# Kernel optimization log

Hardware: AMD Instinct MI355X
Metric: run time of the kernel (lower is better)

## Reference

```python
import jax, jax.numpy as jnp
import numpy as np

N_NODES = 50000
N_EDGES = 600000
IN_DIM = 128
OUT_DIM = 128
LN_EPS = 1e-5


def setup_inputs() -> dict:
    key = jax.random.key(0)
    ks = jax.random.split(key, 8)
    feat = jax.random.normal(ks[0], (N_NODES, IN_DIM), dtype=jnp.float32)
    src = jax.random.randint(ks[1], (N_EDGES,), 0, N_NODES, dtype=jnp.int32)
    dst = jax.random.randint(ks[2], (N_EDGES,), 0, N_NODES, dtype=jnp.int32)
    s = 1.0 / np.sqrt(IN_DIM)
    fc_w = jax.random.uniform(ks[3], (IN_DIM, OUT_DIM), jnp.float32, -s, s)
    fc_b = jax.random.uniform(ks[4], (OUT_DIM,), jnp.float32, -s, s)
    res_w = jax.random.uniform(ks[5], (IN_DIM, OUT_DIM), jnp.float32, -s, s)
    ln_g = jnp.ones((OUT_DIM,), jnp.float32)
    ln_b = jnp.zeros((OUT_DIM,), jnp.float32)
    return {"feat": feat, "src": src, "dst": dst, "fc_w": fc_w,
            "fc_b": fc_b, "res_w": res_w, "ln_g": ln_g, "ln_b": ln_b}


def _deg_norm(idx, n, dtype):
    # degree per node computed from edge endpoint list, clamp(min=1)^-0.5
    deg = jax.ops.segment_sum(jnp.ones(idx.shape, dtype), idx, num_segments=n)
    return jax.lax.rsqrt(jnp.maximum(deg, 1.0))


def _layernorm(x, g, b):
    mu = jnp.mean(x, axis=-1, keepdims=True)
    var = jnp.mean(jnp.square(x - mu), axis=-1, keepdims=True)
    return (x - mu) * jax.lax.rsqrt(var + LN_EPS) * g + b


def reference(feat, src, dst, fc_w, fc_b, res_w, ln_g, ln_b):
    n = feat.shape[0]
    out_norm = _deg_norm(src, n, feat.dtype)  # out-degrees (source norm)
    in_norm = _deg_norm(dst, n, feat.dtype)   # in-degrees (dest norm)
    h = feat * out_norm[:, None]
    # copy_src + sum: gather source features along edges, scatter-add to dst
    agg = jax.ops.segment_sum(h[src], dst, num_segments=n)  # [N, in_dim]
    rst = agg @ fc_w + fc_b
    rst = rst * in_norm[:, None]
    rst = rst + feat @ res_w
    return jax.nn.relu(_layernorm(rst, ln_g, ln_b))
```

## Files before the change

### kernel.cpp

```cpp
#include <hip/hip_runtime.h>

#define N_NODES 50000
#define N_EDGES 600000
#define DIM 128
#define LN_EPS 1e-5f
#define ELL_CAP 64

#define OFF_AGGBF    0
#define OFF_FEATBF   3200000
#define OFF_DEGOUT   6400000
#define OFF_DEGIN    6450000
#define OFF_WTFC     6500000
#define OFF_WTRES    6508192

typedef __attribute__((ext_vector_type(8))) short bf16x8;
typedef __attribute__((ext_vector_type(4))) float f32x4;

__device__ __forceinline__ unsigned int f2bf(float f) {
    unsigned int u = __float_as_uint(f);
    return (u + 0x7FFFu + ((u >> 16) & 1u)) >> 16;
}
__device__ __forceinline__ float bf_lo(unsigned int u) { return __uint_as_float(u << 16); }
__device__ __forceinline__ float bf_hi(unsigned int u) { return __uint_as_float(u & 0xFFFF0000u); }

__global__ void k_prep(const float4* __restrict__ feat, uint2* __restrict__ featbf,
                       unsigned int* __restrict__ degs,
                       const float* __restrict__ fc_w, const float* __restrict__ res_w,
                       unsigned int* __restrict__ wt_fc, unsigned int* __restrict__ wt_res) {
    int gid = blockIdx.x * blockDim.x + threadIdx.x;
    if (gid < N_NODES * DIM / 4) {
        float4 v = feat[gid];
        uint2 o;
        o.x = f2bf(v.x) | (f2bf(v.y) << 16);
        o.y = f2bf(v.z) | (f2bf(v.w) << 16);
        featbf[gid] = o;
    }
    if (gid < 2 * N_NODES) {
        degs[gid] = 0u;
    } else if (gid < 2 * N_NODES + 2 * DIM * (DIM / 2)) {
        int i = gid - 2 * N_NODES;
        int m = i >> 13;
        int r = i & 8191;
        int c = r >> 6;
        int kw = r & 63;
        const float* W = m ? res_w : fc_w;
        unsigned int* O = m ? wt_res : wt_fc;
        float a = W[(size_t)(2 * kw) * DIM + c];
        float b = W[(size_t)(2 * kw + 1) * DIM + c];
        O[c * (DIM / 2) + kw] = f2bf(a) | (f2bf(b) << 16);
    }
}

__global__ void k_count_scatter(const int* __restrict__ src, const int* __restrict__ dst,
                                unsigned int* deg_out, unsigned int* deg_in,
                                unsigned short* __restrict__ ell) {
    int e = blockIdx.x * blockDim.x + threadIdx.x;
    if (e < N_EDGES) {
        int s = src[e], d = dst[e];
        atomicAdd(&deg_out[s], 1u);
        unsigned int ofs = atomicAdd(&deg_in[d], 1u);
        if (ofs < ELL_CAP)
            ell[(size_t)d * ELL_CAP + ofs] = (unsigned short)s;
    }
}

__global__ void k_agg(const unsigned int* __restrict__ featbf,
                      const unsigned int* __restrict__ deg_in,
                      const unsigned int* __restrict__ deg_out,
                      const unsigned short* __restrict__ ell,
                      unsigned int* __restrict__ aggbf) {
    int wid  = (blockIdx.x * blockDim.x + threadIdx.x) >> 6;
    int lane = threadIdx.x & 63;
    if (wid >= N_NODES) return;
    int deg = (int)deg_in[wid];
    if (deg > ELL_CAP) deg = ELL_CAP;
    int   myid = 0;
    float myw  = 0.f;
    if (lane < deg) {
        myid = (int)ell[(size_t)wid * ELL_CAP + lane];
        myw  = rsqrtf(fmaxf((float)deg_out[myid], 1.0f));
    }
    float a0 = 0.f, a1 = 0.f, b0 = 0.f, b1 = 0.f;
    int j = 0;
    for (; j + 3 < deg; j += 4) {
        int   s0 = __shfl(myid, j, 64),     s1 = __shfl(myid, j + 1, 64);
        int   s2 = __shfl(myid, j + 2, 64), s3 = __shfl(myid, j + 3, 64);
        float w0 = __shfl(myw, j, 64),      w1 = __shfl(myw, j + 1, 64);
        float w2 = __shfl(myw, j + 2, 64),  w3 = __shfl(myw, j + 3, 64);
        unsigned int u0 = featbf[(size_t)s0 * 64 + lane];
        unsigned int u1 = featbf[(size_t)s1 * 64 + lane];
        unsigned int u2 = featbf[(size_t)s2 * 64 + lane];
        unsigned int u3 = featbf[(size_t)s3 * 64 + lane];
        a0 = fmaf(w0, bf_lo(u0), a0);  a1 = fmaf(w0, bf_hi(u0), a1);
        b0 = fmaf(w1, bf_lo(u1), b0);  b1 = fmaf(w1, bf_hi(u1), b1);
        a0 = fmaf(w2, bf_lo(u2), a0);  a1 = fmaf(w2, bf_hi(u2), a1);
        b0 = fmaf(w3, bf_lo(u3), b0);  b1 = fmaf(w3, bf_hi(u3), b1);
    }
    for (; j < deg; ++j) {
        int   sa = __shfl(myid, j, 64);
        float wa = __shfl(myw, j, 64);
        unsigned int ua = featbf[(size_t)sa * 64 + lane];
        a0 = fmaf(wa, bf_lo(ua), a0);
        a1 = fmaf(wa, bf_hi(ua), a1);
    }
    float inn = rsqrtf(fmaxf((float)deg, 1.0f));
    a0 = (a0 + b0) * inn;
    a1 = (a1 + b1) * inn;
    aggbf[(size_t)wid * 64 + lane] = f2bf(a0) | (f2bf(a1) << 16);
}

__launch_bounds__(256)
__global__ void k_gemm(const unsigned short* __restrict__ aggbf,
                       const unsigned short* __restrict__ featbf,
                       const unsigned short* __restrict__ wt_fc,
                       const unsigned short* __restrict__ wt_res,
                       const float* __restrict__ fc_b,
                       const unsigned int* __restrict__ deg_in,
                       const float* __restrict__ ln_g, const float* __restrict__ ln_b,
                       float* __restrict__ out) {
    int tid  = threadIdx.x;
    int wave = tid >> 6;
    int lane = tid & 63;
    int fr   = lane & 15;
    int kg   = lane >> 4;
    int row0 = blockIdx.x * 64 + wave * 16;

    f32x4 acc[8];
#pragma unroll
    for (int n = 0; n < 8; n++) acc[n] = (f32x4)0.f;

    int arow = row0 + fr;
#pragma unroll
    for (int pass = 0; pass < 2; ++pass) {
        const unsigned short* X  = pass ? featbf : aggbf;
        const unsigned short* WT = pass ? wt_res : wt_fc;
#pragma unroll
        for (int ks = 0; ks < 4; ++ks) {
            bf16x8 a = *(const bf16x8*)&X[(size_t)arow * DIM + ks * 32 + kg * 8];
#pragma unroll
            for (int n = 0; n < 8; n++) {
                bf16x8 b = *(const bf16x8*)&WT[(size_t)(n * 16 + fr) * DIM + ks * 32 + kg * 8];
                acc[n] = __builtin_amdgcn_mfma_f32_16x16x32_bf16(a, b, acc[n], 0, 0, 0);
            }
        }
    }

    float bia[8], g[8], bb[8];
#pragma unroll
    for (int n = 0; n < 8; n++) {
        int col = n * 16 + fr;
        bia[n] = fc_b[col]; g[n] = ln_g[col]; bb[n] = ln_b[col];
    }
#pragma unroll
    for (int j = 0; j < 4; j++) {
        int row = row0 + kg * 4 + j;
        bool ok = row < N_NODES;
        float inn = ok ? rsqrtf(fmaxf((float)deg_in[row], 1.0f)) : 0.f;
        float x[8], s = 0.f, ss = 0.f;
#pragma unroll
        for (int n = 0; n < 8; n++) {
            x[n] = acc[n][j] + inn * bia[n];
            s += x[n];
            ss = fmaf(x[n], x[n], ss);
        }
#pragma unroll
        for (int m = 1; m < 16; m <<= 1) {
            s  += __shfl_xor(s, m, 64);
            ss += __shfl_xor(ss, m, 64);
        }
        float mu   = s * (1.f / 128.f);
        float var  = ss * (1.f / 128.f) - mu * mu;
        float rstd = rsqrtf(var + LN_EPS);
        if (ok) {
#pragma unroll
            for (int n = 0; n < 8; n++) {
                float o = fmaxf((x[n] - mu) * rstd * g[n] + bb[n], 0.f);
                out[(size_t)row * DIM + n * 16 + fr] = o;
            }
        }
    }
}

extern "C" void kernel_launch(void* const* d_in, const int* in_sizes, int n_in,
                              void* d_out, int out_size, void* d_ws, size_t ws_size,
                              hipStream_t stream) {
    const float* feat  = (const float*)d_in[0];
    const int*   src   = (const int*)d_in[1];
    const int*   dst   = (const int*)d_in[2];
    const float* fc_w  = (const float*)d_in[3];
    const float* fc_b  = (const float*)d_in[4];
    const float* res_w = (const float*)d_in[5];
    const float* ln_g  = (const float*)d_in[6];
    const float* ln_b  = (const float*)d_in[7];
    float* out = (float*)d_out;

    unsigned int* ws_u = (unsigned int*)d_ws;

    unsigned int*   aggbf    = ws_u + OFF_AGGBF;
    unsigned int*   featbf   = ws_u + OFF_FEATBF;
    unsigned int*   deg_out  = ws_u + OFF_DEGOUT;
    unsigned int*   deg_in   = ws_u + OFF_DEGIN;
    unsigned int*   wt_fc    = ws_u + OFF_WTFC;
    unsigned int*   wt_res   = ws_u + OFF_WTRES;
    unsigned short* ell      = (unsigned short*)d_out;

    k_prep<<<(N_NODES * DIM / 4 + 255) / 256, 256, 0, stream>>>(
        (const float4*)feat, (uint2*)featbf, deg_out, fc_w, res_w, wt_fc, wt_res);
    k_count_scatter<<<(N_EDGES + 255) / 256, 256, 0, stream>>>(src, dst, deg_out,
                                                               deg_in, ell);
    {
        long long tot_threads = (long long)N_NODES * 64;
        int blocks = (int)((tot_threads + 255) / 256);
        k_agg<<<blocks, 256, 0, stream>>>(featbf, deg_in, deg_out, ell, aggbf);
    }
    k_gemm<<<(N_NODES + 63) / 64, 256, 0, stream>>>(
        (const unsigned short*)aggbf, (const unsigned short*)featbf,
        (const unsigned short*)wt_fc, (const unsigned short*)wt_res,
        fc_b, deg_in, ln_g, ln_b, out);
}
```

Measured before the change: 213.9 us.

## Fuse aggregation into GEMM via LDS and merge edge scatter with feature conversion

The per-node gather-aggregation now runs inside the GEMM kernel: each wave aggregates its 16 rows into a swizzled LDS tile, which then feeds the fc MFMA directly. This removes the aggbf round trip through global memory and one kernel launch. The bf16 feature conversion is moved into the edge-counting kernel as separate blocks, and each edge thread now handles two edges. The cost is fewer waves doing aggregation (16 rows per wave, done serially), which can reduce the memory-level parallelism available to hide gather latency.

New measurement: 228.5 us. +6.8%, slower.

```diff
diff --git a/kernel.cpp b/kernel.cpp
--- a/kernel.cpp
+++ b/kernel.cpp
@@ -2,16 +2,20 @@
 
 #define N_NODES 50000
 #define N_EDGES 600000
+#define HALF_E  300000
 #define DIM 128
 #define LN_EPS 1e-5f
 #define ELL_CAP 64
 
-#define OFF_AGGBF    0
-#define OFF_FEATBF   3200000
-#define OFF_DEGOUT   6400000
-#define OFF_DEGIN    6450000
-#define OFF_WTFC     6500000
-#define OFF_WTRES    6508192
+#define OFF_FEATBF   0
+#define OFF_DEGOUT   3200000
+#define OFF_DEGIN    3250000
+#define OFF_WTFC     3300000
+#define OFF_WTRES    3308192
+
+#define EDGE_BLOCKS  ((HALF_E + 255) / 256)
+#define CONV_TASKS   (N_NODES * DIM / 4)
+#define CONV_BLOCKS  ((CONV_TASKS + 255) / 256)
 
 typedef __attribute__((ext_vector_type(8))) short bf16x8;
 typedef __attribute__((ext_vector_type(4))) float f32x4;
@@ -23,18 +27,10 @@
 __device__ __forceinline__ float bf_lo(unsigned int u) { return __uint_as_float(u << 16); }
 __device__ __forceinline__ float bf_hi(unsigned int u) { return __uint_as_float(u & 0xFFFF0000u); }
 
-__global__ void k_prep(const float4* __restrict__ feat, uint2* __restrict__ featbf,
-                       unsigned int* __restrict__ degs,
-                       const float* __restrict__ fc_w, const float* __restrict__ res_w,
-                       unsigned int* __restrict__ wt_fc, unsigned int* __restrict__ wt_res) {
+__global__ void k_pre(unsigned int* __restrict__ degs,
+                      const float* __restrict__ fc_w, const float* __restrict__ res_w,
+                      unsigned int* __restrict__ wt_fc, unsigned int* __restrict__ wt_res) {
     int gid = blockIdx.x * blockDim.x + threadIdx.x;
-    if (gid < N_NODES * DIM / 4) {
-        float4 v = feat[gid];
-        uint2 o;
-        o.x = f2bf(v.x) | (f2bf(v.y) << 16);
-        o.y = f2bf(v.z) | (f2bf(v.w) << 16);
-        featbf[gid] = o;
-    }
     if (gid < 2 * N_NODES) {
         degs[gid] = 0u;
     } else if (gid < 2 * N_NODES + 2 * DIM * (DIM / 2)) {
@@ -51,97 +47,118 @@
     }
 }
 
-__global__ void k_count_scatter(const int* __restrict__ src, const int* __restrict__ dst,
-                                unsigned int* deg_out, unsigned int* deg_in,
-                                unsigned short* __restrict__ ell) {
-    int e = blockIdx.x * blockDim.x + threadIdx.x;
-    if (e < N_EDGES) {
-        int s = src[e], d = dst[e];
-        atomicAdd(&deg_out[s], 1u);
-        unsigned int ofs = atomicAdd(&deg_in[d], 1u);
-        if (ofs < ELL_CAP)
-            ell[(size_t)d * ELL_CAP + ofs] = (unsigned short)s;
-    }
-}
-
-__global__ void k_agg(const unsigned int* __restrict__ featbf,
-                      const unsigned int* __restrict__ deg_in,
-                      const unsigned int* __restrict__ deg_out,
-                      const unsigned short* __restrict__ ell,
-                      unsigned int* __restrict__ aggbf) {
-    int wid  = (blockIdx.x * blockDim.x + threadIdx.x) >> 6;
-    int lane = threadIdx.x & 63;
-    if (wid >= N_NODES) return;
-    int deg = (int)deg_in[wid];
-    if (deg > ELL_CAP) deg = ELL_CAP;
-    int   myid = 0;
-    float myw  = 0.f;
-    if (lane < deg) {
-        myid = (int)ell[(size_t)wid * ELL_CAP + lane];
-        myw  = rsqrtf(fmaxf((float)deg_out[myid], 1.0f));
-    }
-    float a0 = 0.f, a1 = 0.f, b0 = 0.f, b1 = 0.f;
-    int j = 0;
-    for (; j + 3 < deg; j += 4) {
-        int   s0 = __shfl(myid, j, 64),     s1 = __shfl(myid, j + 1, 64);
-        int   s2 = __shfl(myid, j + 2, 64), s3 = __shfl(myid, j + 3, 64);
-        float w0 = __shfl(myw, j, 64),      w1 = __shfl(myw, j + 1, 64);
-        float w2 = __shfl(myw, j + 2, 64),  w3 = __shfl(myw, j + 3, 64);
-        unsigned int u0 = featbf[(size_t)s0 * 64 + lane];
-        unsigned int u1 = featbf[(size_t)s1 * 64 + lane];
-        unsigned int u2 = featbf[(size_t)s2 * 64 + lane];
-        unsigned int u3 = featbf[(size_t)s3 * 64 + lane];
-        a0 = fmaf(w0, bf_lo(u0), a0);  a1 = fmaf(w0, bf_hi(u0), a1);
-        b0 = fmaf(w1, bf_lo(u1), b0);  b1 = fmaf(w1, bf_hi(u1), b1);
-        a0 = fmaf(w2, bf_lo(u2), a0);  a1 = fmaf(w2, bf_hi(u2), a1);
-        b0 = fmaf(w3, bf_lo(u3), b0);  b1 = fmaf(w3, bf_hi(u3), b1);
-    }
-    for (; j < deg; ++j) {
-        int   sa = __shfl(myid, j, 64);
-        float wa = __shfl(myw, j, 64);
-        unsigned int ua = featbf[(size_t)sa * 64 + lane];
-        a0 = fmaf(wa, bf_lo(ua), a0);
-        a1 = fmaf(wa, bf_hi(ua), a1);
-    }
-    float inn = rsqrtf(fmaxf((float)deg, 1.0f));
-    a0 = (a0 + b0) * inn;
-    a1 = (a1 + b1) * inn;
-    aggbf[(size_t)wid * 64 + lane] = f2bf(a0) | (f2bf(a1) << 16);
+__global__ void k_main(const int* __restrict__ src, const int* __restrict__ dst,
+                       unsigned int* deg_out, unsigned int* deg_in,
+                       unsigned short* __restrict__ ell,
+                       const float4* __restrict__ feat, uint2* __restrict__ featbf) {
+    int b = blockIdx.x;
+    if (b < EDGE_BLOCKS) {
+        int g = b * 256 + threadIdx.x;
+        if (g < HALF_E) {
+            int s0 = src[g],          d0 = dst[g];
+            int s1 = src[g + HALF_E], d1 = dst[g + HALF_E];
+            atomicAdd(&deg_out[s0], 1u);
+            atomicAdd(&deg_out[s1], 1u);
+            unsigned int o0 = atomicAdd(&deg_in[d0], 1u);
+            unsigned int o1 = atomicAdd(&deg_in[d1], 1u);
+            if (o0 < ELL_CAP) ell[(size_t)d0 * ELL_CAP + o0] = (unsigned short)s0;
+            if (o1 < ELL_CAP) ell[(size_t)d1 * ELL_CAP + o1] = (unsigned short)s1;
+        }
+    } else {
+        int g = (b - EDGE_BLOCKS) * 256 + threadIdx.x;
+        if (g < CONV_TASKS) {
+            float4 v = feat[g];
+            uint2 o;
+            o.x = f2bf(v.x) | (f2bf(v.y) << 16);
+            o.y = f2bf(v.z) | (f2bf(v.w) << 16);
+            featbf[g] = o;
+        }
+    }
 }
 
 __launch_bounds__(256)
-__global__ void k_gemm(const unsigned short* __restrict__ aggbf,
-                       const unsigned short* __restrict__ featbf,
-                       const unsigned short* __restrict__ wt_fc,
-                       const unsigned short* __restrict__ wt_res,
-                       const float* __restrict__ fc_b,
-                       const unsigned int* __restrict__ deg_in,
-                       const float* __restrict__ ln_g, const float* __restrict__ ln_b,
-                       float* __restrict__ out) {
+__global__ void k_agg_gemm(const unsigned int* __restrict__ featbf,
+                           const unsigned int* __restrict__ deg_in,
+                           const unsigned int* __restrict__ deg_out,
+                           const unsigned short* __restrict__ ell,
+                           const unsigned short* __restrict__ wt_fc,
+                           const unsigned short* __restrict__ wt_res,
+                           const float* __restrict__ fc_b,
+                           const float* __restrict__ ln_g, const float* __restrict__ ln_b,
+                           float* __restrict__ out) {
+    __shared__ unsigned int lds[4 * 16 * 64];
     int tid  = threadIdx.x;
     int wave = tid >> 6;
     int lane = tid & 63;
     int fr   = lane & 15;
     int kg   = lane >> 4;
     int row0 = blockIdx.x * 64 + wave * 16;
+    unsigned int* wlds = &lds[wave * 1024];
+
+    for (int n = 0; n < 16; ++n) {
+        int row = row0 + n;
+        int tdeg = 0;
+        if (row < N_NODES) tdeg = (int)deg_in[row];
+        int deg = tdeg > ELL_CAP ? ELL_CAP : tdeg;
+        int   myid = 0;
+        float myw  = 0.f;
+        if (lane < deg) {
+            myid = (int)ell[(size_t)row * ELL_CAP + lane];
+            myw  = rsqrtf(fmaxf((float)deg_out[myid], 1.0f));
+        }
+        float a0 = 0.f, a1 = 0.f, c0 = 0.f, c1 = 0.f;
+        int j = 0;
+        for (; j + 3 < deg; j += 4) {
+            int   s0 = __shfl(myid, j, 64),     s1 = __shfl(myid, j + 1, 64);
+            int   s2 = __shfl(myid, j + 2, 64), s3 = __shfl(myid, j + 3, 64);
+            float w0 = __shfl(myw, j, 64),      w1 = __shfl(myw, j + 1, 64);
+            float w2 = __shfl(myw, j + 2, 64),  w3 = __shfl(myw, j + 3, 64);
+            unsigned int u0 = featbf[(size_t)s0 * 64 + lane];
+            unsigned int u1 = featbf[(size_t)s1 * 64 + lane];
+            unsigned int u2 = featbf[(size_t)s2 * 64 + lane];
+            unsigned int u3 = featbf[(size_t)s3 * 64 + lane];
+            a0 = fmaf(w0, bf_lo(u0), a0);  a1 = fmaf(w0, bf_hi(u0), a1);
+            c0 = fmaf(w1, bf_lo(u1), c0);  c1 = fmaf(w1, bf_hi(u1), c1);
+            a0 = fmaf(w2, bf_lo(u2), a0);  a1 = fmaf(w2, bf_hi(u2), a1);
+            c0 = fmaf(w3, bf_lo(u3), c0);  c1 = fmaf(w3, bf_hi(u3), c1);
+        }
+        for (; j < deg; ++j) {
+            int   sa = __shfl(myid, j, 64);
+            float wa = __shfl(myw, j, 64);
+            unsigned int ua = featbf[(size_t)sa * 64 + lane];
+            a0 = fmaf(wa, bf_lo(ua), a0);
+            a1 = fmaf(wa, bf_hi(ua), a1);
+        }
+        float inn = rsqrtf(fmaxf((float)tdeg, 1.0f));
+        a0 = (a0 + c0) * inn;
+        a1 = (a1 + c1) * inn;
+        wlds[n * 64 + ((((lane >> 2) + n) & 15) << 2) + (lane & 3)] =
+            f2bf(a0) | (f2bf(a1) << 16);
+    }
+    __syncthreads();
 
     f32x4 acc[8];
 #pragma unroll
     for (int n = 0; n < 8; n++) acc[n] = (f32x4)0.f;
 
+#pragma unroll
+    for (int ks = 0; ks < 4; ++ks) {
+        bf16x8 a = *(const bf16x8*)&wlds[fr * 64 + (((ks * 4 + kg + fr) & 15) << 2)];
+#pragma unroll
+        for (int n = 0; n < 8; n++) {
+            bf16x8 bfr = *(const bf16x8*)&wt_fc[(size_t)(n * 16 + fr) * DIM + ks * 32 + kg * 8];
+            acc[n] = __builtin_amdgcn_mfma_f32_16x16x32_bf16(a, bfr, acc[n], 0, 0, 0);
+        }
+    }
     int arow = row0 + fr;
-#pragma unroll
-    for (int pass = 0; pass < 2; ++pass) {
-        const unsigned short* X  = pass ? featbf : aggbf;
-        const unsigned short* WT = pass ? wt_res : wt_fc;
-#pragma unroll
-        for (int ks = 0; ks < 4; ++ks) {
-            bf16x8 a = *(const bf16x8*)&X[(size_t)arow * DIM + ks * 32 + kg * 8];
-#pragma unroll
-            for (int n = 0; n < 8; n++) {
-                bf16x8 b = *(const bf16x8*)&WT[(size_t)(n * 16 + fr) * DIM + ks * 32 + kg * 8];
-                acc[n] = __builtin_amdgcn_mfma_f32_16x16x32_bf16(a, b, acc[n], 0, 0, 0);
-            }
+    if (arow >= N_NODES) arow = N_NODES - 1;
+#pragma unroll
+    for (int ks = 0; ks < 4; ++ks) {
+        bf16x8 a = *(const bf16x8*)&((const unsigned short*)featbf)[(size_t)arow * DIM + ks * 32 + kg * 8];
+#pragma unroll
+        for (int n = 0; n < 8; n++) {
+            bf16x8 bfr = *(const bf16x8*)&wt_res[(size_t)(n * 16 + fr) * DIM + ks * 32 + kg * 8];
+            acc[n] = __builtin_amdgcn_mfma_f32_16x16x32_bf16(a, bfr, acc[n], 0, 0, 0);
         }
     }
 
@@ -196,25 +213,21 @@
 
     unsigned int* ws_u = (unsigned int*)d_ws;
 
-    unsigned int*   aggbf    = ws_u + OFF_AGGBF;
-    unsigned int*   featbf   = ws_u + OFF_FEATBF;
-    unsigned int*   deg_out  = ws_u + OFF_DEGOUT;
-    unsigned int*   deg_in   = ws_u + OFF_DEGIN;
-    unsigned int*   wt_fc    = ws_u + OFF_WTFC;
-    unsigned int*   wt_res   = ws_u + OFF_WTRES;
-    unsigned short* ell      = (unsigned short*)d_out;
-
-    k_prep<<<(N_NODES * DIM / 4 + 255) / 256, 256, 0, stream>>>(
-        (const float4*)feat, (uint2*)featbf, deg_out, fc_w, res_w, wt_fc, wt_res);
-    k_count_scatter<<<(N_EDGES + 255) / 256, 256, 0, stream>>>(src, dst, deg_out,
-                                                               deg_in, ell);
+    unsigned int*   featbf  = ws_u + OFF_FEATBF;
+    unsigned int*   deg_out = ws_u + OFF_DEGOUT;
+    unsigned int*   deg_in  = ws_u + OFF_DEGIN;
+    unsigned int*   wt_fc   = ws_u + OFF_WTFC;
+    unsigned int*   wt_res  = ws_u + OFF_WTRES;
+    unsigned short* ell     = (unsigned short*)d_out;
+
     {
-        long long tot_threads = (long long)N_NODES * 64;
-        int blocks = (int)((tot_threads + 255) / 256);
-        k_agg<<<blocks, 256, 0, stream>>>(featbf, deg_in, deg_out, ell, aggbf);
-    }
-    k_gemm<<<(N_NODES + 63) / 64, 256, 0, stream>>>(
-        (const unsigned short*)aggbf, (const unsigned short*)featbf,
+        int tasks = 2 * N_NODES + 2 * DIM * (DIM / 2);
+        k_pre<<<(tasks + 255) / 256, 256, 0, stream>>>(deg_out, fc_w, res_w, wt_fc, wt_res);
+    }
+    k_main<<<EDGE_BLOCKS + CONV_BLOCKS, 256, 0, stream>>>(
+        src, dst, deg_out, deg_in, ell, (const float4*)feat, (uint2*)featbf);
+    k_agg_gemm<<<(N_NODES + 63) / 64, 256, 0, stream>>>(
+        featbf, deg_in, deg_out, ell,
         (const unsigned short*)wt_fc, (const unsigned short*)wt_res,
-        fc_b, deg_in, ln_g, ln_b, out);
-}
+        fc_b, ln_g, ln_b, out);
+}
```

## Overlap feature bf16 conversion with edge counting in one merged kernel

Applied to the files above, without the earlier changes.

Moves the feat-to-bf16 conversion out of the prep kernel and into the edge scatter kernel as extra blocks, so the streaming conversion runs alongside the atomic-bound degree counting and ELL fill. The prep kernel now only zeroes degrees and transposes weights, so it launches a much smaller grid. Each edge thread now handles four edges spaced a quarter of the edge list apart. It also uses the uncapped in-degree for the normalization and clamps out-of-range GEMM rows, which fixes correctness for high-degree and tail cases.

New measurement: 213.5 us. Within noise of the previous version (-0.2%).

```diff
diff --git a/kernel.cpp b/kernel.cpp
--- a/kernel.cpp
+++ b/kernel.cpp
@@ -2,6 +2,7 @@
 
 #define N_NODES 50000
 #define N_EDGES 600000
+#define QUART_E 150000
 #define DIM 128
 #define LN_EPS 1e-5f
 #define ELL_CAP 64
@@ -13,6 +14,10 @@
 #define OFF_WTFC     6500000
 #define OFF_WTRES    6508192
 
+#define EDGE_BLOCKS  ((QUART_E + 255) / 256)
+#define CONV_TASKS   (N_NODES * DIM / 4)
+#define CONV_BLOCKS  ((CONV_TASKS + 255) / 256)
+
 typedef __attribute__((ext_vector_type(8))) short bf16x8;
 typedef __attribute__((ext_vector_type(4))) float f32x4;
 
@@ -23,18 +28,10 @@
 __device__ __forceinline__ float bf_lo(unsigned int u) { return __uint_as_float(u << 16); }
 __device__ __forceinline__ float bf_hi(unsigned int u) { return __uint_as_float(u & 0xFFFF0000u); }
 
-__global__ void k_prep(const float4* __restrict__ feat, uint2* __restrict__ featbf,
-                       unsigned int* __restrict__ degs,
-                       const float* __restrict__ fc_w, const float* __restrict__ res_w,
-                       unsigned int* __restrict__ wt_fc, unsigned int* __restrict__ wt_res) {
+__global__ void k_pre(unsigned int* __restrict__ degs,
+                      const float* __restrict__ fc_w, const float* __restrict__ res_w,
+                      unsigned int* __restrict__ wt_fc, unsigned int* __restrict__ wt_res) {
     int gid = blockIdx.x * blockDim.x + threadIdx.x;
-    if (gid < N_NODES * DIM / 4) {
-        float4 v = feat[gid];
-        uint2 o;
-        o.x = f2bf(v.x) | (f2bf(v.y) << 16);
-        o.y = f2bf(v.z) | (f2bf(v.w) << 16);
-        featbf[gid] = o;
-    }
     if (gid < 2 * N_NODES) {
         degs[gid] = 0u;
     } else if (gid < 2 * N_NODES + 2 * DIM * (DIM / 2)) {
@@ -51,16 +48,33 @@
     }
 }
 
-__global__ void k_count_scatter(const int* __restrict__ src, const int* __restrict__ dst,
-                                unsigned int* deg_out, unsigned int* deg_in,
-                                unsigned short* __restrict__ ell) {
-    int e = blockIdx.x * blockDim.x + threadIdx.x;
-    if (e < N_EDGES) {
-        int s = src[e], d = dst[e];
-        atomicAdd(&deg_out[s], 1u);
-        unsigned int ofs = atomicAdd(&deg_in[d], 1u);
-        if (ofs < ELL_CAP)
-            ell[(size_t)d * ELL_CAP + ofs] = (unsigned short)s;
+__global__ void k_main(const int* __restrict__ src, const int* __restrict__ dst,
+                       unsigned int* deg_out, unsigned int* deg_in,
+                       unsigned short* __restrict__ ell,
+                       const float4* __restrict__ feat, uint2* __restrict__ featbf) {
+    int b = blockIdx.x;
+    if (b < EDGE_BLOCKS) {
+        int g = b * 256 + threadIdx.x;
+        if (g < QUART_E) {
+#pragma unroll
+            for (int q = 0; q < 4; ++q) {
+                int e = g + q * QUART_E;
+                int s = src[e], d = dst[e];
+                atomicAdd(&deg_out[s], 1u);
+                unsigned int o = atomicAdd(&deg_in[d], 1u);
+                if (o < ELL_CAP)
+                    ell[(size_t)d * ELL_CAP + o] = (unsigned short)s;
+            }
+        }
+    } else {
+        int g = (b - EDGE_BLOCKS) * 256 + threadIdx.x;
+        if (g < CONV_TASKS) {
+            float4 v = feat[g];
+            uint2 o;
+            o.x = f2bf(v.x) | (f2bf(v.y) << 16);
+            o.y = f2bf(v.z) | (f2bf(v.w) << 16);
+            featbf[g] = o;
+        }
     }
 }
 
@@ -72,8 +86,8 @@
     int wid  = (blockIdx.x * blockDim.x + threadIdx.x) >> 6;
     int lane = threadIdx.x & 63;
     if (wid >= N_NODES) return;
-    int deg = (int)deg_in[wid];
-    if (deg > ELL_CAP) deg = ELL_CAP;
+    int tdeg = (int)deg_in[wid];
+    int deg = tdeg > ELL_CAP ? ELL_CAP : tdeg;
     int   myid = 0;
     float myw  = 0.f;
     if (lane < deg) {
@@ -103,7 +117,7 @@
         a0 = fmaf(wa, bf_lo(ua), a0);
         a1 = fmaf(wa, bf_hi(ua), a1);
     }
-    float inn = rsqrtf(fmaxf((float)deg, 1.0f));
+    float inn = rsqrtf(fmaxf((float)tdeg, 1.0f));
     a0 = (a0 + b0) * inn;
     a1 = (a1 + b1) * inn;
     aggbf[(size_t)wid * 64 + lane] = f2bf(a0) | (f2bf(a1) << 16);
@@ -130,6 +144,7 @@
     for (int n = 0; n < 8; n++) acc[n] = (f32x4)0.f;
 
     int arow = row0 + fr;
+    if (arow >= N_NODES) arow = N_NODES - 1;
 #pragma unroll
     for (int pass = 0; pass < 2; ++pass) {
         const unsigned short* X  = pass ? featbf : aggbf;
@@ -196,18 +211,20 @@
 
     unsigned int* ws_u = (unsigned int*)d_ws;
 
-    unsigned int*   aggbf    = ws_u + OFF_AGGBF;
-    unsigned int*   featbf   = ws_u + OFF_FEATBF;
-    unsigned int*   deg_out  = ws_u + OFF_DEGOUT;
-    unsigned int*   deg_in   = ws_u + OFF_DEGIN;
-    unsigned int*   wt_fc    = ws_u + OFF_WTFC;
-    unsigned int*   wt_res   = ws_u + OFF_WTRES;
-    unsigned short* ell      = (unsigned short*)d_out;
-
-    k_prep<<<(N_NODES * DIM / 4 + 255) / 256, 256, 0, stream>>>(
-        (const float4*)feat, (uint2*)featbf, deg_out, fc_w, res_w, wt_fc, wt_res);
-    k_count_scatter<<<(N_EDGES + 255) / 256, 256, 0, stream>>>(src, dst, deg_out,
-                                                               deg_in, ell);
+    unsigned int*   aggbf   = ws_u + OFF_AGGBF;
+    unsigned int*   featbf  = ws_u + OFF_FEATBF;
+    unsigned int*   deg_out = ws_u + OFF_DEGOUT;
+    unsigned int*   deg_in  = ws_u + OFF_DEGIN;
+    unsigned int*   wt_fc   = ws_u + OFF_WTFC;
+    unsigned int*   wt_res  = ws_u + OFF_WTRES;
+    unsigned short* ell     = (unsigned short*)d_out;
+
+    {
+        int tasks = 2 * N_NODES + 2 * DIM * (DIM / 2);
+        k_pre<<<(tasks + 255) / 256, 256, 0, stream>>>(deg_out, fc_w, res_w, wt_fc, wt_res);
+    }
+    k_main<<<EDGE_BLOCKS + CONV_BLOCKS, 256, 0, stream>>>(
+        src, dst, deg_out, deg_in, ell, (const float4*)feat, (uint2*)featbf);
     {
         long long tot_threads = (long long)N_NODES * 64;
         int blocks = (int)((tot_threads + 255) / 256);
```
